# Performance work log

Hardware: AMD Instinct MI355X
Metric: run time of the kernel (lower is better)

Reference implementation:

```python
import jax, jax.numpy as jnp
import numpy as np

TOP_K = 2
N_EXPERTS = 8
N_EMBED = 1024
B, T = 4, 1024


def setup_inputs() -> dict:
    key = jax.random.key(0)
    k1, k2, k3 = jax.random.split(key, 3)
    x = jax.random.normal(k1, (B, T, N_EMBED), dtype=jnp.float32)
    wg_kernel = jax.random.normal(k2, (N_EMBED, N_EXPERTS), dtype=jnp.float32) * 0.02
    wg_bias = jnp.zeros((N_EXPERTS,), dtype=jnp.float32)
    # Experts.__call__ only uses w_c_fc: (E, C, C), stddev 0.02
    w_c_fc = jax.random.normal(k3, (N_EXPERTS, N_EMBED, N_EMBED), dtype=jnp.float32) * 0.02
    return {"x": x, "wg_kernel": wg_kernel, "wg_bias": wg_bias, "w_c_fc": w_c_fc}


def _dispatch(xb, logits, n_experts, top_k):
    # xb: (T, C), logits: (T, E)
    T, C = xb.shape
    top_k_logits, idx = jax.lax.top_k(logits, top_k)          # (T, k)
    probs = jax.nn.softmax(top_k_logits, axis=-1)             # (T, k)
    flat_idx = jnp.swapaxes(idx, 0, 1).ravel()                # (k*T,), k-major order
    one_hot = jax.nn.one_hot(flat_idx, n_experts, dtype=jnp.int32)
    pos = jnp.cumsum(one_hot, axis=0) * one_hot - 1           # running slot per expert
    pos = jnp.swapaxes(pos.reshape(top_k, T, n_experts), 0, 1).max(axis=2)  # (T, k)
    idx_tk = jnp.swapaxes(flat_idx.reshape(top_k, T), 0, 1)   # (T, k)
    cap = top_k * T
    x_rep = jnp.repeat(xb, top_k, axis=0)                     # (T*k, C), token-major
    buf = jnp.zeros((n_experts, cap, C), xb.dtype)
    buf = buf.at[idx_tk.ravel(), pos.ravel()].add(x_rep)      # scatter dispatch
    return probs, pos, idx_tk, buf


def reference(x, wg_kernel, wg_bias, w_c_fc):
    Bb, Tt, C = x.shape
    n_experts = w_c_fc.shape[0]
    logits = x @ wg_kernel + wg_bias                           # (B, T, E)
    probs, pos, idx, buf = jax.vmap(
        lambda xb, lb: _dispatch(xb, lb, n_experts, TOP_K))(x, logits)
    # buf: (B, E, cap, C). The original's reshape/swapaxes shuffle is a pure
    # permutation of the (B, cap) token axis that is exactly inverted after the
    # expert GEMM, so it is mathematically a no-op; apply the grouped GEMM directly.
    out = jnp.einsum('beti,eio->beto', buf, w_c_fc)            # per-expert matmul
    gathered = jax.vmap(lambda o, i, p: o[i, p])(out, idx, pos)  # (B, T, k, C)
    y = jnp.einsum('btkc,btk->btc', gathered, probs)
    return y, probs
```

## Files before the change

### kernel.cpp

```cpp
#include <hip/hip_runtime.h>
#include <math.h>

typedef __attribute__((ext_vector_type(8))) __bf16 bf16x8;
typedef __attribute__((ext_vector_type(4))) __bf16 bf16x4v;
typedef __attribute__((ext_vector_type(16))) float f32x16;

#define N_TOK  4096
#define C_DIM  1024
#define N_EXP  8
#define CAP    4096

#define WS_CNT    0
#define WS_PERM   32768
#define WS_XB     ((size_t)1 << 20)
#define WS_WT     (WS_XB + ((size_t)8 << 20))

#define GLD16(g, l)                                                        \
  __builtin_amdgcn_global_load_lds(                                        \
      (const __attribute__((address_space(1))) void*)(g),                  \
      (__attribute__((address_space(3))) void*)(l), 16, 0, 0)

__global__ __launch_bounds__(256)
void prep_kernel(const float* __restrict__ x, const float* __restrict__ wg,
                 const float* __restrict__ bias, const float* __restrict__ W,
                 __bf16* __restrict__ xb, float* __restrict__ probs,
                 __bf16* __restrict__ Wt, int* __restrict__ cnt,
                 int* __restrict__ perm) {
  __shared__ __align__(16) char smem[32768];
  __shared__ int lcnt[N_EXP], base[N_EXP];
  const int tid = threadIdx.x;

  if (blockIdx.x < 256) {
    float (*wgT)[C_DIM] = (float (*)[C_DIM])smem;
    if (tid < N_EXP) lcnt[tid] = 0;

#pragma unroll
    for (int i = 0; i < 8; ++i) {
      const float4 v = ((const float4*)wg)[i * 256 + tid];
      const int f = (i * 256 + tid) * 4;
      const int c = f >> 3;
      const int e = f & 7;
      wgT[e][c] = v.x; wgT[e + 1][c] = v.y; wgT[e + 2][c] = v.z; wgT[e + 3][c] = v.w;
    }
    __syncthreads();

    const int lane = tid & 63;
    const int wv   = tid >> 6;
    int re0[4], re1[4], rs0[4], rs1[4];

#pragma unroll
    for (int s = 0; s < 4; ++s) {
      const int t = blockIdx.x * 16 + wv * 4 + s;
      const float4* xrow = (const float4*)(x + (size_t)t * C_DIM);
      float acc[N_EXP];
#pragma unroll
      for (int e = 0; e < N_EXP; ++e) acc[e] = 0.f;

#pragma unroll
      for (int j = 0; j < 4; ++j) {
        const int c4 = j * 64 + lane;
        const float4 v = xrow[c4];
        bf16x4v bv = { (__bf16)v.x, (__bf16)v.y, (__bf16)v.z, (__bf16)v.w };
        *(bf16x4v*)(xb + (size_t)t * C_DIM + c4 * 4) = bv;
#pragma unroll
        for (int e = 0; e < N_EXP; ++e) {
          const float4 w = *(const float4*)&wgT[e][c4 * 4];
          acc[e] += v.x * w.x + v.y * w.y + v.z * w.z + v.w * w.w;
        }
      }

#pragma unroll
      for (int off = 32; off >= 1; off >>= 1) {
#pragma unroll
        for (int e = 0; e < N_EXP; ++e) acc[e] += __shfl_xor(acc[e], off, 64);
      }

      if (lane == 0) {
        float l[N_EXP];
#pragma unroll
        for (int e = 0; e < N_EXP; ++e) l[e] = acc[e] + bias[e];
        int e0 = 0;
#pragma unroll
        for (int e = 1; e < N_EXP; ++e) if (l[e] > l[e0]) e0 = e;
        int e1 = (e0 == 0) ? 1 : 0;
#pragma unroll
        for (int e = 0; e < N_EXP; ++e) if (e != e0 && l[e] > l[e1]) e1 = e;
        const float p0 = 1.f / (1.f + expf(l[e1] - l[e0]));
        probs[t * 2]     = p0;
        probs[t * 2 + 1] = 1.f - p0;
        re0[s] = e0; re1[s] = e1;
        rs0[s] = atomicAdd(&lcnt[e0], 1);
        rs1[s] = atomicAdd(&lcnt[e1], 1);
      }
    }
    __syncthreads();
    if (tid < N_EXP) base[tid] = atomicAdd(&cnt[tid], lcnt[tid]);
    __syncthreads();
    if (lane == 0) {
#pragma unroll
      for (int s = 0; s < 4; ++s) {
        const int t = blockIdx.x * 16 + wv * 4 + s;
        perm[re0[s] * CAP + base[re0[s]] + rs0[s]] = t * 2;
        perm[re1[s] * CAP + base[re1[s]] + rs1[s]] = t * 2 + 1;
      }
    }
  } else {
    __bf16 (*tile)[33] = (__bf16 (*)[33])smem;
    const int b  = blockIdx.x - 256;
    const int e  = b >> 10;
    const int r  = b & 1023;
    const int i0 = (r >> 5) * 32;
    const int o0 = (r & 31) * 32;
    const float* We  = W  + (size_t)e * C_DIM * C_DIM;
    __bf16*      Wte = Wt + (size_t)e * C_DIM * C_DIM;
    const int tx = tid & 31, ty = tid >> 5;
#pragma unroll
    for (int j = 0; j < 32; j += 8)
      tile[ty + j][tx] = (__bf16)We[(size_t)(i0 + ty + j) * C_DIM + o0 + tx];
    __syncthreads();
#pragma unroll
    for (int j = 0; j < 32; j += 8)
      Wte[(size_t)(o0 + ty + j) * C_DIM + i0 + tx] = tile[tx][ty + j];
  }
}

__global__ __launch_bounds__(512)
void moe_gemm(const __bf16* __restrict__ xb, const __bf16* __restrict__ Wt,
              const int* __restrict__ cnt, const int* __restrict__ perm,
              __bf16* __restrict__ buf) {
  const int gid = blockIdx.x;
  const int e   = gid & 7;
  const int n0  = ((gid >> 3) & 7) * 128;
  const int m0  = (gid >> 6) * 128;
  const int count = cnt[e];
  if (m0 >= count) return;

  const int*    permE = perm + e * CAP;
  const __bf16* We    = Wt + (size_t)e * C_DIM * C_DIM;

  __shared__ __align__(16) char smem[32768];

  const int tid  = threadIdx.x;
  const int lane = tid & 63;
  const int wv   = tid >> 6;
  const int wr = wv >> 1, wc = wv & 1;
  const int l32 = lane & 31, hi = lane >> 5;

  const int rsub  = lane >> 3;
  const int chunk = (lane & 7) ^ rsub;

  int tk[2];
#pragma unroll
  for (int q = 0; q < 2; ++q) {
    const int i = m0 + wv * 16 + q * 8 + rsub;
    tk[q] = (i < count) ? (permE[i] >> 1) : 0;
  }
  const char* gA = (const char*)xb;
  const char* gB = (const char*)We + (size_t)(n0 + wv * 16 + rsub) * 2048 +
                   chunk * 16;

  f32x16 acc[2];
#pragma unroll
  for (int ng = 0; ng < 2; ++ng)
#pragma unroll
    for (int r = 0; r < 16; ++r) acc[ng][r] = 0.f;

  for (int kt = 0; kt < 16; ++kt) {
    const int kb = kt * 128;
    {
      char* lA = smem + (wv * 16) * 128;
      char* lB = smem + 16384 + (wv * 16) * 128;
#pragma unroll
      for (int q = 0; q < 2; ++q)
        GLD16(gA + (size_t)tk[q] * 2048 + kb + chunk * 16, lA + q * 1024);
#pragma unroll
      for (int q = 0; q < 2; ++q)
        GLD16(gB + (size_t)q * 8 * 2048 + kb, lB + q * 1024);
    }
    __syncthreads();

#pragma unroll
    for (int ks = 0; ks < 4; ++ks) {
      const int c = ks * 2 + hi;
      const int rA = wr * 32 + l32;
      const bf16x8 af = *(const bf16x8*)(smem + rA * 128 + ((c ^ (rA & 7)) << 4));
      bf16x8 bfr[2];
#pragma unroll
      for (int ng = 0; ng < 2; ++ng) {
        const int rB = wc * 64 + ng * 32 + l32;
        bfr[ng] = *(const bf16x8*)(smem + 16384 + rB * 128 + ((c ^ (rB & 7)) << 4));
      }
#pragma unroll
      for (int ng = 0; ng < 2; ++ng)
        acc[ng] = __builtin_amdgcn_mfma_f32_32x32x16_bf16(af, bfr[ng], acc[ng], 0, 0, 0);
    }
    __syncthreads();
  }

#pragma unroll
  for (int r = 0; r < 16; ++r) {
    const int row = (r & 3) + 8 * (r >> 2) + 4 * hi;
    const int i = m0 + wr * 32 + row;
    if (i < count) {
      const int pe = permE[i];
      __bf16* orow = buf + (size_t)(pe >> 1) * 2048 + (pe & 1) * 1024 +
                     n0 + wc * 64 + l32;
      orow[0]  = (__bf16)acc[0][r];
      orow[32] = (__bf16)acc[1][r];
    }
  }
}

__global__ __launch_bounds__(256)
void combine(const float* __restrict__ probs, float* __restrict__ y) {
  const int t = blockIdx.x;
  const int c = threadIdx.x * 4;
  const __bf16* bt = (const __bf16*)(y + (size_t)t * C_DIM);
  const bf16x4v b0 = *(const bf16x4v*)(bt + c);
  const bf16x4v b1 = *(const bf16x4v*)(bt + 1024 + c);
  const float p0 = probs[2 * t], p1 = probs[2 * t + 1];
  __syncthreads();
  float4 o = { p0 * (float)b0[0] + p1 * (float)b1[0],
               p0 * (float)b0[1] + p1 * (float)b1[1],
               p0 * (float)b0[2] + p1 * (float)b1[2],
               p0 * (float)b0[3] + p1 * (float)b1[3] };
  *(float4*)(y + (size_t)t * C_DIM + c) = o;
}

extern "C" void kernel_launch(void* const* d_in, const int* in_sizes, int n_in,
                              void* d_out, int out_size, void* d_ws, size_t ws_size,
                              hipStream_t stream) {
  const float* x    = (const float*)d_in[0];
  const float* wg   = (const float*)d_in[1];
  const float* bias = (const float*)d_in[2];
  const float* wcfc = (const float*)d_in[3];

  float* y     = (float*)d_out;
  float* probs = y + (size_t)N_TOK * C_DIM;
  __bf16* buf  = (__bf16*)d_out;

  char* ws   = (char*)d_ws;
  int*    cnt  = (int*)(ws + WS_CNT);
  int*    perm = (int*)(ws + WS_PERM);
  __bf16* xb   = (__bf16*)(ws + WS_XB);
  __bf16* Wt   = (__bf16*)(ws + WS_WT);

  hipMemsetAsync(cnt, 0, N_EXP * sizeof(int), stream);

  prep_kernel<<<256 + 8192, 256, 0, stream>>>(x, wg, bias, wcfc, xb, probs,
                                              Wt, cnt, perm);
  moe_gemm<<<8 * 8 * 32, 512, 0, stream>>>(xb, Wt, cnt, perm, buf);
  combine<<<N_TOK, 256, 0, stream>>>(probs, y);
}
```

Measured before the change: 136.2 us.

## Double-buffer LDS tiles in MoE GEMM to overlap loads with MFMA

The expert GEMM now has two 32 KB LDS buffers. Each iteration issues the global-to-LDS loads for the next K tile before running the MFMAs on the current one, so memory latency can hide behind compute. The cost is twice the LDS per block, which may lower occupancy. It also relies on the single barrier per iteration being enough to make the async loads visible.

```diff
diff --git a/kernel.cpp b/kernel.cpp
--- a/kernel.cpp
+++ b/kernel.cpp
@@ -138,7 +138,7 @@
   const int*    permE = perm + e * CAP;
   const __bf16* We    = Wt + (size_t)e * C_DIM * C_DIM;
 
-  __shared__ __align__(16) char smem[32768];
+  __shared__ __align__(16) char smem[65536];
 
   const int tid  = threadIdx.x;
   const int lane = tid & 63;
@@ -165,37 +165,47 @@
 #pragma unroll
     for (int r = 0; r < 16; ++r) acc[ng][r] = 0.f;
 
+#define STAGE(bufsel, kb)                                                    \
+  do {                                                                       \
+    char* lA = smem + (bufsel) * 32768 + (wv * 16) * 128;                    \
+    char* lB = lA + 16384;                                                   \
+    _Pragma("unroll")                                                        \
+    for (int q = 0; q < 2; ++q)                                              \
+      GLD16(gA + (size_t)tk[q] * 2048 + (kb) + chunk * 16, lA + q * 1024);   \
+    _Pragma("unroll")                                                        \
+    for (int q = 0; q < 2; ++q)                                              \
+      GLD16(gB + (size_t)q * 8 * 2048 + (kb), lB + q * 1024);                \
+  } while (0)
+
+  STAGE(0, 0);
+  __syncthreads();
+
+  int cur = 0;
   for (int kt = 0; kt < 16; ++kt) {
-    const int kb = kt * 128;
-    {
-      char* lA = smem + (wv * 16) * 128;
-      char* lB = smem + 16384 + (wv * 16) * 128;
-#pragma unroll
-      for (int q = 0; q < 2; ++q)
-        GLD16(gA + (size_t)tk[q] * 2048 + kb + chunk * 16, lA + q * 1024);
-#pragma unroll
-      for (int q = 0; q < 2; ++q)
-        GLD16(gB + (size_t)q * 8 * 2048 + kb, lB + q * 1024);
-    }
-    __syncthreads();
-
+    const int nxt = cur ^ 1;
+    if (kt < 15) STAGE(nxt, (kt + 1) * 128);
+
+    const char* Ab = smem + cur * 32768;
+    const char* Bb = Ab + 16384;
 #pragma unroll
     for (int ks = 0; ks < 4; ++ks) {
       const int c = ks * 2 + hi;
       const int rA = wr * 32 + l32;
-      const bf16x8 af = *(const bf16x8*)(smem + rA * 128 + ((c ^ (rA & 7)) << 4));
+      const bf16x8 af = *(const bf16x8*)(Ab + rA * 128 + ((c ^ (rA & 7)) << 4));
       bf16x8 bfr[2];
 #pragma unroll
       for (int ng = 0; ng < 2; ++ng) {
         const int rB = wc * 64 + ng * 32 + l32;
-        bfr[ng] = *(const bf16x8*)(smem + 16384 + rB * 128 + ((c ^ (rB & 7)) << 4));
+        bfr[ng] = *(const bf16x8*)(Bb + rB * 128 + ((c ^ (rB & 7)) << 4));
       }
 #pragma unroll
       for (int ng = 0; ng < 2; ++ng)
         acc[ng] = __builtin_amdgcn_mfma_f32_32x32x16_bf16(af, bfr[ng], acc[ng], 0, 0, 0);
     }
     __syncthreads();
-  }
+    cur = nxt;
+  }
+#undef STAGE
 
 #pragma unroll
   for (int r = 0; r < 16; ++r) {
```

Result: slower. 142.4 us (+4.6%).

## Replace global atomic slot allocation with per-block counts and prefix-scan perm build

Applied to the files above, without the earlier changes.

The routing blocks now record per-block, per-expert local counts and token lists instead of reserving global slots with atomics, and a new small kernel runs a prefix scan over the block counts to build the per-expert permutation in token order. This removes the memset and the global atomics, and makes the permutation deterministic. In exchange it adds an extra kernel launch with a serial copy loop per thread, and the local lists are sized for at most 32 entries per block and expert.

```diff
diff --git a/kernel.cpp b/kernel.cpp
--- a/kernel.cpp
+++ b/kernel.cpp
@@ -11,7 +11,9 @@
 #define CAP    4096
 
 #define WS_CNT    0
+#define WS_CNTS   4096
 #define WS_PERM   32768
+#define WS_LOC    262144
 #define WS_XB     ((size_t)1 << 20)
 #define WS_WT     (WS_XB + ((size_t)8 << 20))
 
@@ -24,10 +26,10 @@
 void prep_kernel(const float* __restrict__ x, const float* __restrict__ wg,
                  const float* __restrict__ bias, const float* __restrict__ W,
                  __bf16* __restrict__ xb, float* __restrict__ probs,
-                 __bf16* __restrict__ Wt, int* __restrict__ cnt,
-                 int* __restrict__ perm) {
+                 __bf16* __restrict__ Wt, int* __restrict__ cnts,
+                 int* __restrict__ loc) {
   __shared__ __align__(16) char smem[32768];
-  __shared__ int lcnt[N_EXP], base[N_EXP];
+  __shared__ int lcnt[N_EXP];
   const int tid = threadIdx.x;
 
   if (blockIdx.x < 256) {
@@ -46,7 +48,6 @@
 
     const int lane = tid & 63;
     const int wv   = tid >> 6;
-    int re0[4], re1[4], rs0[4], rs1[4];
 
 #pragma unroll
     for (int s = 0; s < 4; ++s) {
@@ -88,22 +89,14 @@
         const float p0 = 1.f / (1.f + expf(l[e1] - l[e0]));
         probs[t * 2]     = p0;
         probs[t * 2 + 1] = 1.f - p0;
-        re0[s] = e0; re1[s] = e1;
-        rs0[s] = atomicAdd(&lcnt[e0], 1);
-        rs1[s] = atomicAdd(&lcnt[e1], 1);
-      }
-    }
-    __syncthreads();
-    if (tid < N_EXP) base[tid] = atomicAdd(&cnt[tid], lcnt[tid]);
-    __syncthreads();
-    if (lane == 0) {
-#pragma unroll
-      for (int s = 0; s < 4; ++s) {
-        const int t = blockIdx.x * 16 + wv * 4 + s;
-        perm[re0[s] * CAP + base[re0[s]] + rs0[s]] = t * 2;
-        perm[re1[s] * CAP + base[re1[s]] + rs1[s]] = t * 2 + 1;
-      }
-    }
+        const int rs0 = atomicAdd(&lcnt[e0], 1);
+        const int rs1 = atomicAdd(&lcnt[e1], 1);
+        loc[(blockIdx.x * N_EXP + e0) * 32 + rs0] = t * 2;
+        loc[(blockIdx.x * N_EXP + e1) * 32 + rs1] = t * 2 + 1;
+      }
+    }
+    __syncthreads();
+    if (tid < N_EXP) cnts[blockIdx.x * N_EXP + tid] = lcnt[tid];
   } else {
     __bf16 (*tile)[33] = (__bf16 (*)[33])smem;
     const int b  = blockIdx.x - 256;
@@ -122,6 +115,28 @@
     for (int j = 0; j < 32; j += 8)
       Wte[(size_t)(o0 + ty + j) * C_DIM + i0 + tx] = tile[tx][ty + j];
   }
+}
+
+__global__ __launch_bounds__(256)
+void build_perm(const int* __restrict__ cnts, const int* __restrict__ loc,
+                int* __restrict__ cnt, int* __restrict__ perm) {
+  const int e = blockIdx.x;
+  const int t = threadIdx.x;
+  __shared__ int sc[256];
+  const int v = cnts[t * N_EXP + e];
+  sc[t] = v;
+  __syncthreads();
+#pragma unroll
+  for (int off = 1; off < 256; off <<= 1) {
+    const int xval = (t >= off) ? sc[t - off] : 0;
+    __syncthreads();
+    sc[t] += xval;
+    __syncthreads();
+  }
+  const int base = sc[t] - v;
+  if (t == 255) cnt[e] = sc[255];
+  const int* src = loc + (t * N_EXP + e) * 32;
+  for (int j = 0; j < v; ++j) perm[e * CAP + base + j] = src[j];
 }
 
 __global__ __launch_bounds__(512)
@@ -241,14 +256,15 @@
 
   char* ws   = (char*)d_ws;
   int*    cnt  = (int*)(ws + WS_CNT);
+  int*    cnts = (int*)(ws + WS_CNTS);
   int*    perm = (int*)(ws + WS_PERM);
+  int*    loc  = (int*)(ws + WS_LOC);
   __bf16* xb   = (__bf16*)(ws + WS_XB);
   __bf16* Wt   = (__bf16*)(ws + WS_WT);
 
-  hipMemsetAsync(cnt, 0, N_EXP * sizeof(int), stream);
-
   prep_kernel<<<256 + 8192, 256, 0, stream>>>(x, wg, bias, wcfc, xb, probs,
-                                              Wt, cnt, perm);
+                                              Wt, cnts, loc);
+  build_perm<<<N_EXP, 256, 0, stream>>>(cnts, loc, cnt, perm);
   moe_gemm<<<8 * 8 * 32, 512, 0, stream>>>(xb, Wt, cnt, perm, buf);
   combine<<<N_TOK, 256, 0, stream>>>(probs, y);
 }
```

Measured after the change: 140.5 us. 1.03x slower.
